# Kernel optimization log

Hardware: AMD Instinct MI355X
Metric: run time of the kernel (lower is better)

Reference implementation:

```python
import jax, jax.numpy as jnp
import numpy as np

D_MODEL = 1024
NUM_HEADS = 8
HEAD_DIM = D_MODEL // NUM_HEADS  # 128


def setup_inputs() -> dict:
    key = jax.random.key(0)
    ks = jax.random.split(key, 11)
    B, S = 2, 2048
    inp = {
        "query": jax.random.normal(ks[0], (B, S, D_MODEL), dtype=jnp.float32),
        "key": jax.random.normal(ks[1], (B, S, D_MODEL), dtype=jnp.float32),
        "value": jax.random.normal(ks[2], (B, S, D_MODEL), dtype=jnp.float32),
        # Dense layer params (Keras Dense: y = x @ W + b), glorot-ish scale
        "Wq": jax.random.normal(ks[3], (D_MODEL, D_MODEL), dtype=jnp.float32) * (1.0 / np.sqrt(D_MODEL)),
        "bq": jnp.zeros((D_MODEL,), dtype=jnp.float32),
        "Wk": jax.random.normal(ks[4], (D_MODEL, D_MODEL), dtype=jnp.float32) * (1.0 / np.sqrt(D_MODEL)),
        "bk": jnp.zeros((D_MODEL,), dtype=jnp.float32),
        "Wv": jax.random.normal(ks[5], (D_MODEL, D_MODEL), dtype=jnp.float32) * (1.0 / np.sqrt(D_MODEL)),
        "bv": jnp.zeros((D_MODEL,), dtype=jnp.float32),
        "Wo": jax.random.normal(ks[6], (D_MODEL, D_MODEL), dtype=jnp.float32) * (1.0 / np.sqrt(D_MODEL)),
        "bo": jnp.zeros((D_MODEL,), dtype=jnp.float32),
    }
    return inp


def _split_heads(x, B):
    # [B, S, D] -> [B, H, S, Hd]
    S = x.shape[1]
    return x.reshape(B, S, NUM_HEADS, HEAD_DIM).transpose(0, 2, 1, 3)


def reference(query, key, value, Wq, bq, Wk, bk, Wv, bv, Wo, bo):
    B, S, _ = query.shape
    q = _split_heads(query @ Wq + bq, B)   # [B,H,S,Hd]
    k = _split_heads(key @ Wk + bk, B)
    v = _split_heads(value @ Wv + bv, B)
    # ReLU (non-softmax) attention; scale by sqrt(per-head dk)
    scale = 1.0 / jnp.sqrt(jnp.float32(HEAD_DIM))
    score = jnp.einsum("bhqd,bhkd->bhqk", q, k) * scale  # [B,H,S,S]
    attn_weights = jax.nn.relu(score)
    # dropout inactive at inference (training=None)
    context = jnp.einsum("bhqk,bhkd->bhqd", attn_weights, v)  # [B,H,S,Hd]
    context = context.transpose(0, 2, 1, 3).reshape(B, S, D_MODEL)
    output = context @ Wo + bo
    return (output, attn_weights)
```

## Files before the change

kernel.cpp:

```cpp
#include <hip/hip_runtime.h>
#include <hip/hip_bf16.h>
#include <stdint.h>

#define D_MODEL 1024
#define NHEAD 8
#define HDIM 128
#define BATCH 2
#define SEQ 2048
#define MTOT (BATCH*SEQ)
#define KVBLK 64
#define NT (SEQ/KVBLK)

typedef __attribute__((ext_vector_type(4))) float f32x4;
typedef __attribute__((ext_vector_type(8))) short bf16x8;

__device__ __forceinline__ uint32_t swz128(uint32_t row, uint32_t cb) {
  return row * 128u + (cb ^ ((row & 7u) << 4));
}
__device__ __forceinline__ uint32_t swz256(uint32_t row, uint32_t cb) {
  return row * 256u + (cb ^ ((row & 7u) << 4));
}

__device__ __forceinline__ void gload16(void* lds, const void* g) {
  __builtin_amdgcn_global_load_lds(
      reinterpret_cast<const __attribute__((address_space(1))) uint32_t*>(
          reinterpret_cast<uintptr_t>(g)),
      reinterpret_cast<__attribute__((address_space(3))) uint32_t*>(
          (uint32_t)reinterpret_cast<uintptr_t>(lds)),
      16, 0, 0);
}

__device__ __forceinline__ void barrier_lgkm() {
  asm volatile("s_waitcnt lgkmcnt(0)\n\ts_barrier" ::: "memory");
}
__device__ __forceinline__ void barrier_vm16() {
  asm volatile("s_waitcnt vmcnt(16) lgkmcnt(0)\n\ts_barrier" ::: "memory");
}
__device__ __forceinline__ void barrier_vm0() {
  asm volatile("s_waitcnt vmcnt(0) lgkmcnt(0)\n\ts_barrier" ::: "memory");
}

__global__ __launch_bounds__(256)
void prep(const float* __restrict__ q, const float* __restrict__ k,
          const float* __restrict__ v, __hip_bfloat16* __restrict__ qkv_out,
          const float* __restrict__ w0, const float* __restrict__ w1,
          const float* __restrict__ w2, const float* __restrict__ w3,
          __hip_bfloat16* __restrict__ t0, __hip_bfloat16* __restrict__ t1,
          __hip_bfloat16* __restrict__ t2, __hip_bfloat16* __restrict__ t3) {
  const int bid = blockIdx.x;
  const int tid = threadIdx.x;
  if (bid < 6144) {
    const int which = bid >> 11;
    const int blk = bid & 2047;
    const float* src = which == 0 ? q : (which == 1 ? k : v);
    const size_t NE = (size_t)MTOT * D_MODEL;
    size_t i = ((size_t)blk * 256 + tid) * 8;
    float4 a = *reinterpret_cast<const float4*>(src + i);
    float4 b = *reinterpret_cast<const float4*>(src + i + 4);
    __hip_bfloat16 o[8] = {__float2bfloat16(a.x), __float2bfloat16(a.y),
                           __float2bfloat16(a.z), __float2bfloat16(a.w),
                           __float2bfloat16(b.x), __float2bfloat16(b.y),
                           __float2bfloat16(b.z), __float2bfloat16(b.w)};
    *reinterpret_cast<uint4*>(qkv_out + which * NE + i) =
        *reinterpret_cast<const uint4*>(o);
  } else {
    const int rb = bid - 6144;
    const int z = rb >> 10;
    const int rem = rb & 1023;
    const float* W = z == 0 ? w0 : z == 1 ? w1 : z == 2 ? w2 : w3;
    __hip_bfloat16* Wt = z == 0 ? t0 : z == 1 ? t1 : z == 2 ? t2 : t3;
    __shared__ float t[32][33];
    const int x = tid & 31, y = tid >> 5;
    const int n0 = (rem & 31) * 32, k0 = (rem >> 5) * 32;
#pragma unroll
    for (int i = 0; i < 4; ++i)
      t[y + i * 8][x] = W[(size_t)(k0 + y + i * 8) * D_MODEL + n0 + x];
    __syncthreads();
#pragma unroll
    for (int i = 0; i < 4; ++i)
      Wt[(size_t)(n0 + y + i * 8) * D_MODEL + k0 + x] = __float2bfloat16(t[x][y + i * 8]);
  }
}

struct GemmArgs {
  const __hip_bfloat16* A;
  const __hip_bfloat16* B;
  const float* bias;
  void* out;
  int mode;
};

__global__ __launch_bounds__(256)
void gemm_gl(GemmArgs g0, GemmArgs g1, GemmArgs g2, int K) {
  __shared__ char lds[2][32768];
  GemmArgs ga = blockIdx.z == 0 ? g0 : (blockIdx.z == 1 ? g1 : g2);

  const int tid = threadIdx.x, lane = tid & 63, wid = tid >> 6;
  const int lrow = lane & 15, lko = (lane >> 4) * 8, rbase = (lane >> 4) * 4;
  const int m0 = blockIdx.x * 128, n0 = blockIdx.y * 128;
  const size_t ldb = (size_t)K * 2;

  const int srow = lane >> 3;
  const int sca = ((lane & 7) * 16) ^ (srow << 4);
  const char* Ab = (const char*)ga.A + (size_t)(m0 + wid * 32 + srow) * ldb + sca;
  const char* Bb = (const char*)ga.B + (size_t)(n0 + wid * 32 + srow) * ldb + sca;
  const int sdst = wid * 32 * 128;

  f32x4 acc[4][4];
  const f32x4 fz = {0.f, 0.f, 0.f, 0.f};
#pragma unroll
  for (int m = 0; m < 4; ++m)
#pragma unroll
    for (int n = 0; n < 4; ++n) acc[m][n] = fz;

  const int wm = (wid >> 1) * 64, wn = (wid & 1) * 64;
  const int NKT = K >> 6;

#pragma unroll
  for (int i = 0; i < 4; ++i) {
    gload16(&lds[0][sdst + i * 8 * 128], Ab + (size_t)i * 8 * ldb);
    gload16(&lds[0][16384 + sdst + i * 8 * 128], Bb + (size_t)i * 8 * ldb);
  }
  barrier_vm0();

  for (int kt = 0; kt < NKT; ++kt) {
    const int c = kt & 1;
    if (kt + 1 < NKT) {
      const size_t koff = (size_t)(kt + 1) * 128;
#pragma unroll
      for (int i = 0; i < 4; ++i) {
        gload16(&lds[c ^ 1][sdst + i * 8 * 128], Ab + (size_t)i * 8 * ldb + koff);
        gload16(&lds[c ^ 1][16384 + sdst + i * 8 * 128], Bb + (size_t)i * 8 * ldb + koff);
      }
    }
    const char* lA = lds[c];
    const char* lB = lds[c] + 16384;
#pragma unroll
    for (int kk = 0; kk < 64; kk += 32) {
      bf16x8 af[4], bf[4];
#pragma unroll
      for (int m = 0; m < 4; ++m)
        af[m] = *reinterpret_cast<const bf16x8*>(&lA[swz128(wm + m * 16 + lrow, (kk + lko) * 2)]);
#pragma unroll
      for (int n = 0; n < 4; ++n)
        bf[n] = *reinterpret_cast<const bf16x8*>(&lB[swz128(wn + n * 16 + lrow, (kk + lko) * 2)]);
      __builtin_amdgcn_s_setprio(1);
#pragma unroll
      for (int m = 0; m < 4; ++m)
#pragma unroll
        for (int n = 0; n < 4; ++n)
          acc[m][n] = __builtin_amdgcn_mfma_f32_16x16x32_bf16(af[m], bf[n], acc[m][n], 0, 0, 0);
      __builtin_amdgcn_s_setprio(0);
    }
    barrier_vm0();
  }

  if (ga.mode == 2) {
#pragma unroll
    for (int m = 0; m < 4; ++m)
#pragma unroll
      for (int n = 0; n < 4; ++n) {
        const int col = n0 + wn + n * 16 + lrow;
        const float bv = ga.bias[col];
#pragma unroll
        for (int r = 0; r < 4; ++r) {
          const int row = m0 + wm + m * 16 + rbase + r;
          reinterpret_cast<float*>(ga.out)[(size_t)row * D_MODEL + col] = acc[m][n][r] + bv;
        }
      }
  } else if (ga.mode == 0) {
#pragma unroll
    for (int m = 0; m < 4; ++m)
#pragma unroll
      for (int n = 0; n < 4; ++n) {
        const int col = n0 + wn + n * 16 + lrow;
        const float bv = ga.bias[col];
        const int h = col >> 7, hd = col & 127;
#pragma unroll
        for (int r = 0; r < 4; ++r) {
          const int row = m0 + wm + m * 16 + rbase + r;
          const int b = row >> 11, s = row & 2047;
          reinterpret_cast<__hip_bfloat16*>(ga.out)[((size_t)(b * NHEAD + h) * SEQ + s) * HDIM + hd] =
              __float2bfloat16(acc[m][n][r] + bv);
        }
      }
  } else {
    char* T = lds[0];
#pragma unroll
    for (int m = 0; m < 4; ++m)
#pragma unroll
      for (int n = 0; n < 4; ++n) {
        const int hdl = wn + n * 16 + lrow;
        const float bv = ga.bias[n0 + hdl];
#pragma unroll
        for (int r = 0; r < 4; ++r) {
          const int sl = wm + m * 16 + rbase + r;
          *reinterpret_cast<__hip_bfloat16*>(&T[swz256(hdl, sl * 2)]) =
              __float2bfloat16(acc[m][n][r] + bv);
        }
      }
    __syncthreads();
    const int b = m0 >> 11, h = n0 >> 7;
    char* vtb = (char*)ga.out +
                (((size_t)(b * NHEAD + h) * HDIM) * SEQ + (m0 & 2047)) * 2;
    const int lr16 = tid >> 4;
    const int lc16 = (tid & 15) * 16;
#pragma unroll
    for (int p = 0; p < 8; ++p) {
      const int hdl = p * 16 + lr16;
      uint4 vv = *reinterpret_cast<const uint4*>(&T[swz256(hdl, lc16)]);
      *reinterpret_cast<uint4*>(vtb + (size_t)hdl * (SEQ * 2) + lc16) = vv;
    }
  }
}

__global__ __launch_bounds__(512)
void attn_v2(const __hip_bfloat16* __restrict__ Qh,
             const __hip_bfloat16* __restrict__ Kh,
             const __hip_bfloat16* __restrict__ Vt,
             float* __restrict__ attn,
             __hip_bfloat16* __restrict__ ctx) {
  __shared__ char ldsK[2][KVBLK * 256];
  __shared__ char ldsV[2][HDIM * 128];
  __shared__ char ldsP[128 * 128];

  const int tid = threadIdx.x, lane = tid & 63, wid = tid >> 6;
  const int lrow = lane & 15, lko = (lane >> 4) * 8, rbase = (lane >> 4) * 4;
  const int wqq = (wid >> 1) * 32;
  const int wqk = (wid & 1) * 32;
  const int whd = (wid & 1) * 64;

  const int raw = blockIdx.x;
  const int xcd = raw & 7, slot = raw >> 3;
  const int bh = xcd * 2 + (slot >> 4);
  const int q0 = (slot & 15) * 128;

  const char* Kg = (const char*)Kh + (size_t)bh * SEQ * HDIM * 2;
  const char* Vg = (const char*)Vt + (size_t)bh * HDIM * SEQ * 2;
  const __hip_bfloat16* Qg = Qh + ((size_t)bh * SEQ + q0) * HDIM;
  float* attnb = attn + ((size_t)bh * SEQ + q0) * SEQ;

  const int krl = lane >> 4;
  const int kcb = (lane & 15) * 16;
  const int vrl = lane >> 3;
  const int vsc = ((lane & 7) * 16) ^ (vrl << 4);

#pragma unroll
  for (int j = 0; j < 2; ++j) {
    const int rr = wid * 8 + j * 4 + krl;
    gload16((char*)ldsK[0] + (wid * 8 + j * 4) * 256,
            Kg + (size_t)rr * 256 + (kcb ^ ((rr & 7) << 4)));
    const int rv = wid * 16 + j * 8 + vrl;
    gload16((char*)ldsV[0] + (wid * 16 + j * 8) * 128,
            Vg + (size_t)rv * (SEQ * 2) + vsc);
  }

  bf16x8 qf[2][4];
#pragma unroll
  for (int m = 0; m < 2; ++m)
#pragma unroll
    for (int kk = 0; kk < 4; ++kk)
      qf[m][kk] = *reinterpret_cast<const bf16x8*>(
          Qg + (size_t)(wqq + m * 16 + lrow) * HDIM + kk * 32 + lko);

  f32x4 cacc[2][4];
  const f32x4 fz = {0.f, 0.f, 0.f, 0.f};
#pragma unroll
  for (int m = 0; m < 2; ++m)
#pragma unroll
    for (int n = 0; n < 4; ++n) cacc[m][n] = fz;

  const float scale = 0.08838834764831845f;
  __syncthreads();

  for (int t = 0; t < NT; ++t) {
    const int b = t & 1;
    if (t + 1 < NT) {
#pragma unroll
      for (int j = 0; j < 2; ++j) {
        const int rr = wid * 8 + j * 4 + krl;
        gload16((char*)ldsK[b ^ 1] + (wid * 8 + j * 4) * 256,
                Kg + (size_t)((t + 1) * KVBLK + rr) * 256 + (kcb ^ ((rr & 7) << 4)));
        const int rv = wid * 16 + j * 8 + vrl;
        gload16((char*)ldsV[b ^ 1] + (wid * 16 + j * 8) * 128,
                Vg + (size_t)rv * (SEQ * 2) + (t + 1) * 128 + vsc);
      }
    }

    f32x4 sacc[2][2];
#pragma unroll
    for (int m = 0; m < 2; ++m)
#pragma unroll
      for (int n = 0; n < 2; ++n) sacc[m][n] = fz;
    __builtin_amdgcn_s_setprio(1);
#pragma unroll
    for (int kk = 0; kk < 4; ++kk) {
      bf16x8 kf[2];
#pragma unroll
      for (int n = 0; n < 2; ++n)
        kf[n] = *reinterpret_cast<const bf16x8*>(
            &ldsK[b][swz256(wqk + n * 16 + lrow, (kk * 32 + lko) * 2)]);
#pragma unroll
      for (int m = 0; m < 2; ++m)
#pragma unroll
        for (int n = 0; n < 2; ++n)
          sacc[m][n] = __builtin_amdgcn_mfma_f32_16x16x32_bf16(qf[m][kk], kf[n], sacc[m][n], 0, 0, 0);
    }
    __builtin_amdgcn_s_setprio(0);

#pragma unroll
    for (int m = 0; m < 2; ++m)
#pragma unroll
      for (int n = 0; n < 2; ++n)
#pragma unroll
        for (int r = 0; r < 4; ++r) {
          const int ql = wqq + m * 16 + rbase + r;
          const int kl = wqk + n * 16 + lrow;
          const float s = fmaxf(sacc[m][n][r] * scale, 0.f);
          attnb[(size_t)ql * SEQ + t * KVBLK + kl] = s;
          *reinterpret_cast<__hip_bfloat16*>(&ldsP[swz128(ql, kl * 2)]) = __float2bfloat16(s);
        }
    barrier_lgkm();

    __builtin_amdgcn_s_setprio(1);
#pragma unroll
    for (int kk = 0; kk < 2; ++kk) {
      bf16x8 pf[2], vf[4];
#pragma unroll
      for (int m = 0; m < 2; ++m)
        pf[m] = *reinterpret_cast<const bf16x8*>(
            &ldsP[swz128(wqq + m * 16 + lrow, (kk * 32 + lko) * 2)]);
#pragma unroll
      for (int n = 0; n < 4; ++n)
        vf[n] = *reinterpret_cast<const bf16x8*>(
            &ldsV[b][swz128(whd + n * 16 + lrow, (kk * 32 + lko) * 2)]);
#pragma unroll
      for (int m = 0; m < 2; ++m)
#pragma unroll
        for (int n = 0; n < 4; ++n)
          cacc[m][n] = __builtin_amdgcn_mfma_f32_16x16x32_bf16(pf[m], vf[n], cacc[m][n], 0, 0, 0);
    }
    __builtin_amdgcn_s_setprio(0);
    barrier_vm16();
  }

  const int bb = bh >> 3, h = bh & 7;
#pragma unroll
  for (int m = 0; m < 2; ++m)
#pragma unroll
    for (int n = 0; n < 4; ++n)
#pragma unroll
      for (int r = 0; r < 4; ++r) {
        const int srow = q0 + wqq + m * 16 + rbase + r;
        const int hd = whd + n * 16 + lrow;
        ctx[((size_t)(bb * SEQ + srow)) * D_MODEL + h * HDIM + hd] =
            __float2bfloat16(cacc[m][n][r]);
      }
}

extern "C" void kernel_launch(void* const* d_in, const int* in_sizes, int n_in,
                              void* d_out, int out_size, void* d_ws, size_t ws_size,
                              hipStream_t stream) {
  const float* q  = (const float*)d_in[0];
  const float* k  = (const float*)d_in[1];
  const float* v  = (const float*)d_in[2];
  const float* Wq = (const float*)d_in[3];
  const float* bq = (const float*)d_in[4];
  const float* Wk = (const float*)d_in[5];
  const float* bk = (const float*)d_in[6];
  const float* Wv = (const float*)d_in[7];
  const float* bv = (const float*)d_in[8];
  const float* Wo = (const float*)d_in[9];
  const float* bo = (const float*)d_in[10];

  char* ws = (char*)d_ws;
  const size_t NE = (size_t)MTOT * D_MODEL;
  const size_t WE = (size_t)D_MODEL * D_MODEL;
  __hip_bfloat16* qb  = (__hip_bfloat16*)ws;
  __hip_bfloat16* kb  = qb + NE;
  __hip_bfloat16* vb  = kb + NE;
  __hip_bfloat16* Wqt = vb + NE;
  __hip_bfloat16* Wkt = Wqt + WE;
  __hip_bfloat16* Wvt = Wkt + WE;
  __hip_bfloat16* Wot = Wvt + WE;
  __hip_bfloat16* Qh  = Wot + WE;
  __hip_bfloat16* Kh  = Qh + NE;
  __hip_bfloat16* Vt  = Kh + NE;
  __hip_bfloat16* ctx = Vt + NE;

  prep<<<10240, 256, 0, stream>>>(q, k, v, qb, Wq, Wk, Wv, Wo, Wqt, Wkt, Wvt, Wot);

  GemmArgs gq{qb, Wqt, bq, Qh, 0};
  GemmArgs gk{kb, Wkt, bk, Kh, 0};
  GemmArgs gv{vb, Wvt, bv, Vt, 1};
  gemm_gl<<<dim3(32, 8, 3), 256, 0, stream>>>(gq, gk, gv, D_MODEL);

  float* outp  = (float*)d_out;
  float* attnp = outp + NE;
  attn_v2<<<256, 512, 0, stream>>>(Qh, Kh, Vt, attnp, ctx);

  GemmArgs go{ctx, Wot, bo, d_out, 2};
  gemm_gl<<<dim3(32, 8, 1), 256, 0, stream>>>(go, go, go, D_MODEL);
}
```

Measured before the change: 147.6 us.

## Double KV tile to 128 and single-buffer V loaded within iteration

The attention kernel now processes 128 keys per iteration instead of 64. This halves the loop trip count and the number of barriers, and gives each wave a wider 32x64 score tile. V is no longer double-buffered. It is loaded into one 256-byte-stride LDS buffer at the start of each iteration and waited on at the mid-iteration barrier through vmcnt(32), while K stays prefetched one tile ahead. This trades V latency hiding, and a stricter wait that also covers the K prefetch, for fewer synchronisations and more MFMA work per barrier. LDS use grows to about 128 KB per block.

```diff
diff --git a/kernel.cpp b/kernel.cpp
--- a/kernel.cpp
+++ b/kernel.cpp
@@ -8,7 +8,7 @@
 #define BATCH 2
 #define SEQ 2048
 #define MTOT (BATCH*SEQ)
-#define KVBLK 64
+#define KVBLK 128
 #define NT (SEQ/KVBLK)
 
 typedef __attribute__((ext_vector_type(4))) float f32x4;
@@ -33,8 +33,8 @@
 __device__ __forceinline__ void barrier_lgkm() {
   asm volatile("s_waitcnt lgkmcnt(0)\n\ts_barrier" ::: "memory");
 }
-__device__ __forceinline__ void barrier_vm16() {
-  asm volatile("s_waitcnt vmcnt(16) lgkmcnt(0)\n\ts_barrier" ::: "memory");
+__device__ __forceinline__ void barrier_vm32() {
+  asm volatile("s_waitcnt vmcnt(32) lgkmcnt(0)\n\ts_barrier" ::: "memory");
 }
 __device__ __forceinline__ void barrier_vm0() {
   asm volatile("s_waitcnt vmcnt(0) lgkmcnt(0)\n\ts_barrier" ::: "memory");
@@ -215,19 +215,19 @@
 }
 
 __global__ __launch_bounds__(512)
-void attn_v2(const __hip_bfloat16* __restrict__ Qh,
+void attn_v6(const __hip_bfloat16* __restrict__ Qh,
              const __hip_bfloat16* __restrict__ Kh,
              const __hip_bfloat16* __restrict__ Vt,
              float* __restrict__ attn,
              __hip_bfloat16* __restrict__ ctx) {
   __shared__ char ldsK[2][KVBLK * 256];
-  __shared__ char ldsV[2][HDIM * 128];
-  __shared__ char ldsP[128 * 128];
+  __shared__ char ldsV[HDIM * 256];
+  __shared__ char ldsP[128 * 256];
 
   const int tid = threadIdx.x, lane = tid & 63, wid = tid >> 6;
   const int lrow = lane & 15, lko = (lane >> 4) * 8, rbase = (lane >> 4) * 4;
   const int wqq = (wid >> 1) * 32;
-  const int wqk = (wid & 1) * 32;
+  const int wqk = (wid & 1) * 64;
   const int whd = (wid & 1) * 64;
 
   const int raw = blockIdx.x;
@@ -240,19 +240,14 @@
   const __hip_bfloat16* Qg = Qh + ((size_t)bh * SEQ + q0) * HDIM;
   float* attnb = attn + ((size_t)bh * SEQ + q0) * SEQ;
 
-  const int krl = lane >> 4;
-  const int kcb = (lane & 15) * 16;
-  const int vrl = lane >> 3;
-  const int vsc = ((lane & 7) * 16) ^ (vrl << 4);
-
-#pragma unroll
-  for (int j = 0; j < 2; ++j) {
-    const int rr = wid * 8 + j * 4 + krl;
-    gload16((char*)ldsK[0] + (wid * 8 + j * 4) * 256,
-            Kg + (size_t)rr * 256 + (kcb ^ ((rr & 7) << 4)));
-    const int rv = wid * 16 + j * 8 + vrl;
-    gload16((char*)ldsV[0] + (wid * 16 + j * 8) * 128,
-            Vg + (size_t)rv * (SEQ * 2) + vsc);
+  const int srl = lane >> 4;
+  const int scb = (lane & 15) * 16;
+
+#pragma unroll
+  for (int j = 0; j < 4; ++j) {
+    const int rr = wid * 16 + j * 4 + srl;
+    gload16((char*)ldsK[0] + (wid * 16 + j * 4) * 256,
+            Kg + (size_t)rr * 256 + (scb ^ ((rr & 7) << 4)));
   }
 
   bf16x8 qf[2][4];
@@ -275,35 +270,38 @@
 
   for (int t = 0; t < NT; ++t) {
     const int b = t & 1;
+#pragma unroll
+    for (int j = 0; j < 4; ++j) {
+      const int rv = wid * 16 + j * 4 + srl;
+      gload16((char*)ldsV + (wid * 16 + j * 4) * 256,
+              Vg + (size_t)rv * (SEQ * 2) + t * 256 + (scb ^ ((rv & 7) << 4)));
+    }
     if (t + 1 < NT) {
 #pragma unroll
-      for (int j = 0; j < 2; ++j) {
-        const int rr = wid * 8 + j * 4 + krl;
-        gload16((char*)ldsK[b ^ 1] + (wid * 8 + j * 4) * 256,
-                Kg + (size_t)((t + 1) * KVBLK + rr) * 256 + (kcb ^ ((rr & 7) << 4)));
-        const int rv = wid * 16 + j * 8 + vrl;
-        gload16((char*)ldsV[b ^ 1] + (wid * 16 + j * 8) * 128,
-                Vg + (size_t)rv * (SEQ * 2) + (t + 1) * 128 + vsc);
-      }
-    }
-
-    f32x4 sacc[2][2];
+      for (int j = 0; j < 4; ++j) {
+        const int rr = wid * 16 + j * 4 + srl;
+        gload16((char*)ldsK[b ^ 1] + (wid * 16 + j * 4) * 256,
+                Kg + (size_t)((t + 1) * KVBLK + rr) * 256 + (scb ^ ((rr & 7) << 4)));
+      }
+    }
+
+    f32x4 sacc[2][4];
 #pragma unroll
     for (int m = 0; m < 2; ++m)
 #pragma unroll
-      for (int n = 0; n < 2; ++n) sacc[m][n] = fz;
+      for (int n = 0; n < 4; ++n) sacc[m][n] = fz;
     __builtin_amdgcn_s_setprio(1);
 #pragma unroll
     for (int kk = 0; kk < 4; ++kk) {
-      bf16x8 kf[2];
-#pragma unroll
-      for (int n = 0; n < 2; ++n)
+      bf16x8 kf[4];
+#pragma unroll
+      for (int n = 0; n < 4; ++n)
         kf[n] = *reinterpret_cast<const bf16x8*>(
             &ldsK[b][swz256(wqk + n * 16 + lrow, (kk * 32 + lko) * 2)]);
 #pragma unroll
       for (int m = 0; m < 2; ++m)
 #pragma unroll
-        for (int n = 0; n < 2; ++n)
+        for (int n = 0; n < 4; ++n)
           sacc[m][n] = __builtin_amdgcn_mfma_f32_16x16x32_bf16(qf[m][kk], kf[n], sacc[m][n], 0, 0, 0);
     }
     __builtin_amdgcn_s_setprio(0);
@@ -311,29 +309,29 @@
 #pragma unroll
     for (int m = 0; m < 2; ++m)
 #pragma unroll
-      for (int n = 0; n < 2; ++n)
+      for (int n = 0; n < 4; ++n)
 #pragma unroll
         for (int r = 0; r < 4; ++r) {
           const int ql = wqq + m * 16 + rbase + r;
           const int kl = wqk + n * 16 + lrow;
           const float s = fmaxf(sacc[m][n][r] * scale, 0.f);
           attnb[(size_t)ql * SEQ + t * KVBLK + kl] = s;
-          *reinterpret_cast<__hip_bfloat16*>(&ldsP[swz128(ql, kl * 2)]) = __float2bfloat16(s);
+          *reinterpret_cast<__hip_bfloat16*>(&ldsP[swz256(ql, kl * 2)]) = __float2bfloat16(s);
         }
-    barrier_lgkm();
+    barrier_vm32();
 
     __builtin_amdgcn_s_setprio(1);
 #pragma unroll
-    for (int kk = 0; kk < 2; ++kk) {
+    for (int kk = 0; kk < 4; ++kk) {
       bf16x8 pf[2], vf[4];
 #pragma unroll
       for (int m = 0; m < 2; ++m)
         pf[m] = *reinterpret_cast<const bf16x8*>(
-            &ldsP[swz128(wqq + m * 16 + lrow, (kk * 32 + lko) * 2)]);
+            &ldsP[swz256(wqq + m * 16 + lrow, (kk * 32 + lko) * 2)]);
 #pragma unroll
       for (int n = 0; n < 4; ++n)
         vf[n] = *reinterpret_cast<const bf16x8*>(
-            &ldsV[b][swz128(whd + n * 16 + lrow, (kk * 32 + lko) * 2)]);
+            &ldsV[swz256(whd + n * 16 + lrow, (kk * 32 + lko) * 2)]);
 #pragma unroll
       for (int m = 0; m < 2; ++m)
 #pragma unroll
@@ -341,7 +339,7 @@
           cacc[m][n] = __builtin_amdgcn_mfma_f32_16x16x32_bf16(pf[m], vf[n], cacc[m][n], 0, 0, 0);
     }
     __builtin_amdgcn_s_setprio(0);
-    barrier_vm16();
+    barrier_lgkm();
   }
 
   const int bb = bh >> 3, h = bh & 7;
@@ -397,7 +395,7 @@
 
   float* outp  = (float*)d_out;
   float* attnp = outp + NE;
-  attn_v2<<<256, 512, 0, stream>>>(Qh, Kh, Vt, attnp, ctx);
+  attn_v6<<<256, 512, 0, stream>>>(Qh, Kh, Vt, attnp, ctx);
 
   GemmArgs go{ctx, Wot, bo, d_out, 2};
   gemm_gl<<<dim3(32, 8, 1), 256, 0, stream>>>(go, go, go, D_MODEL);
```

Measured after the change: 144.1 us. -2.4%, faster.
